# Kernel optimization log

Measured on AMD Instinct MI355X. Metric: run time of the kernel, lower is better.

Reference implementation:

```python
import jax, jax.numpy as jnp
import numpy as np
from jax import lax


def setup_inputs() -> dict:
    key = jax.random.key(0)
    kw, ku, kk, kv = jax.random.split(key, 4)
    B, H, W, C = 8, 16, 16, 256
    # w is a positive per-channel decay (offset keeps exp(sum relu(...)) numerically sane);
    # k, u scaled down like trained RWKV params to avoid exp overflow in the reference.
    w = jax.random.uniform(kw, (C,), dtype=jnp.float32) + 0.3
    u = jax.random.normal(ku, (C,), dtype=jnp.float32) * 0.1
    k = jax.random.normal(kk, (B, H, W, C), dtype=jnp.float32) * 0.1
    v = jax.random.normal(kv, (B, H, W, C), dtype=jnp.float32)
    return {"B": B, "H": H, "W": W, "C": C, "w": w, "u": u, "k": k, "v": v}


def _wkv2d(B, H, W, C, w, u, k, v):
    # kernel covers the whole feature map
    K = 2 * (max(H, W) - 1) + 1
    pad = K // 2
    c = K // 2
    # Manhattan-distance decay weights, (C, K, K), with bonus u at the center.
    coords = jnp.arange(K)
    dist = (jnp.abs(coords[None, :] - c) + jnp.abs(coords[:, None] - c)).astype(w.dtype)
    wmat = -dist[None, :, :] * w[:, None, None]
    wmat = wmat.at[:, c, c].add(u)
    wflat = wmat.reshape(C, K * K).T  # (K*K, C)

    k_chw = jnp.transpose(k, (0, 3, 1, 2))  # (B,C,H,W)
    k_pad = jnp.pad(k_chw, ((0, 0), (0, 0), (pad, pad), (pad, pad)))  # zero pad == F.unfold padding

    idx = jnp.arange(K * K, dtype=jnp.int32)
    dys, dxs = idx // K, idx % K

    # Fused windowed relu-sum: never materialize the (B,C,K^2,HW) unfold tensor.
    def body(acc, xs):
        dy, dx, wc = xs
        win = lax.dynamic_slice(k_pad, (0, 0, dy, dx), (B, C, H, W))
        return acc + jax.nn.relu(win + wc[None, :, None, None]), None

    acc0 = jnp.zeros((B, C, H, W), dtype=k.dtype)
    k_adj, _ = lax.scan(body, acc0, (dys, dxs, wflat))

    v_chw = jnp.transpose(v, (0, 3, 1, 2))
    out = jnp.exp(k_adj) * v_chw  # (B,C,H,W)
    return jnp.transpose(out, (0, 2, 3, 1))  # back to (B,H,W,C)


def reference(B, H, W, C, w, u, k, v):
    return _wkv2d(B, H, W, C, w, u, k, v)
```

## Files before the change

kernel.cpp:

```cpp
#include <hip/hip_runtime.h>
#include <math.h>


constexpr int Bq = 8, Hq = 16, Wq = 16, Cq = 256;
constexpr int HW = Hq * Wq;
constexpr int CG = 16;
constexpr int YT = 2;
constexpr int ROWP = HW + 4;

__global__ __launch_bounds__(256, 4)
void wkv2d_kernel(const float* __restrict__ w,
                  const float* __restrict__ u,
                  const float* __restrict__ k,
                  const float* __restrict__ v,
                  float* __restrict__ out) {
    __shared__ float klds[CG][ROWP];

    const int bid = blockIdx.x;
    const int y0  = (bid & 7) * YT;
    const int c0  = ((bid >> 3) & 15) * CG;
    const int b   = bid >> 7;

    const int tid = threadIdx.x;
    const int cl  = tid & 15;
    const int x   = tid >> 4;

    {
        #pragma unroll
        for (int i = 0; i < 4; ++i) {
            const int f = tid + 256 * i;
            const int p = f >> 2;
            const int q = f & 3;
            const float4 kv = ((const float4*)(k + ((size_t)(b * HW + p)) * Cq + c0))[q];
            klds[4 * q + 0][p] = kv.x;
            klds[4 * q + 1][p] = kv.y;
            klds[4 * q + 2][p] = kv.z;
            klds[4 * q + 3][p] = kv.w;
        }
    }
    __syncthreads();

    const int   c  = c0 + cl;
    const float wc = w[c];
    const float fx = (float)x;
    const float fy0 = (float)y0;

    float wxv[16];
    #pragma unroll
    for (int rx = 0; rx < 16; ++rx)
        wxv[rx] = fabsf((float)rx - fx) * wc;

    float acc0 = 0.f, acc1 = 0.f;
    const float* krow = &klds[cl][0];

    #pragma unroll
    for (int ry = 0; ry < 16; ++ry) {
        const float fy  = (float)ry;
        const float wy0 = fabsf(fy - fy0) * wc;
        const float wy1 = fabsf(fy - fy0 - 1.0f) * wc;

        const float4* rr = (const float4*)(krow + ry * 16);
        #pragma unroll
        for (int j = 0; j < 4; ++j) {
            const float4 r = rr[j];
            const float rv[4] = {r.x, r.y, r.z, r.w};
            #pragma unroll
            for (int t = 0; t < 4; ++t) {
                const float t0 = rv[t] - wxv[4 * j + t];
                acc0 += fmaxf(t0 - wy0, 0.f);
                acc1 += fmaxf(t0 - wy1, 0.f);
            }
        }
    }

    const float uc  = u[c];
    const float ks0 = krow[(y0 + 0) * 16 + x];
    const float ks1 = krow[(y0 + 1) * 16 + x];
    const float a0 = acc0 + fmaxf(ks0 + uc, 0.f) - fmaxf(ks0, 0.f);
    const float a1 = acc1 + fmaxf(ks1 + uc, 0.f) - fmaxf(ks1, 0.f);

    const size_t idx0 = ((size_t)((b * 16 + y0) * 16 + x)) * Cq + c;
    const size_t idx1 = idx0 + (size_t)Wq * Cq;
    out[idx0] = __expf(a0) * v[idx0];
    out[idx1] = __expf(a1) * v[idx1];
}

extern "C" void kernel_launch(void* const* d_in, const int* in_sizes, int n_in,
                              void* d_out, int out_size, void* d_ws, size_t ws_size,
                              hipStream_t stream) {
    const float* w = (const float*)d_in[4];
    const float* u = (const float*)d_in[5];
    const float* k = (const float*)d_in[6];
    const float* v = (const float*)d_in[7];
    float* out = (float*)d_out;

    const int grid = Bq * (Cq / CG) * (Hq / YT);
    wkv2d_kernel<<<grid, 256, 0, stream>>>(w, u, k, v, out);
}
```

Before: 81.62 us.

## Skip zero relu terms by bounding window radius from per-channel k max

Computes the max k per channel in the block and derives the largest Manhattan distance D at which relu(k - d*w) can be positive. When D is small, only a (2D+2)x(2D+1) neighbourhood is summed instead of the whole 16x16 map; otherwise it falls back to the full loop. This cuts ALU work that contributes only zeros, at the cost of an extra reduction, two block barriers and data-dependent, less-unrolled loops.

```diff
diff --git a/kernel.cpp b/kernel.cpp
--- a/kernel.cpp
+++ b/kernel.cpp
@@ -15,6 +15,8 @@
                   const float* __restrict__ v,
                   float* __restrict__ out) {
     __shared__ float klds[CG][ROWP];
+    __shared__ float pmax[CG][17];
+    __shared__ int   sD[CG];
 
     const int bid = blockIdx.x;
     const int y0  = (bid & 7) * YT;
@@ -40,35 +42,88 @@
     }
     __syncthreads();
 
+    {
+        const float4* rr = (const float4*)(&klds[cl][x * 16]);
+        const float4 a = rr[0], bb = rr[1], cc = rr[2], dd = rr[3];
+        float m = fmaxf(fmaxf(fmaxf(a.x, a.y), fmaxf(a.z, a.w)),
+                        fmaxf(fmaxf(bb.x, bb.y), fmaxf(bb.z, bb.w)));
+        m = fmaxf(m, fmaxf(fmaxf(cc.x, cc.y), fmaxf(cc.z, cc.w)));
+        m = fmaxf(m, fmaxf(fmaxf(dd.x, dd.y), fmaxf(dd.z, dd.w)));
+        pmax[cl][x] = m;
+    }
+    __syncthreads();
+
+    if (tid < CG) {
+        float km = pmax[tid][0];
+        #pragma unroll
+        for (int i = 1; i < 16; ++i) km = fmaxf(km, pmax[tid][i]);
+        const float wcc = w[c0 + tid];
+        int D = -1;
+        for (int d = 0; d <= 30; ++d) {
+            if (km > (float)d * wcc - 1e-5f) D = d; else break;
+        }
+        sD[tid] = D;
+    }
+    __syncthreads();
+
+    int Dblk = sD[0];
+    #pragma unroll
+    for (int i = 1; i < 16; ++i) Dblk = max(Dblk, sD[i]);
+
     const int   c  = c0 + cl;
     const float wc = w[c];
     const float fx = (float)x;
     const float fy0 = (float)y0;
 
-    float wxv[16];
-    #pragma unroll
-    for (int rx = 0; rx < 16; ++rx)
-        wxv[rx] = fabsf((float)rx - fx) * wc;
-
     float acc0 = 0.f, acc1 = 0.f;
     const float* krow = &klds[cl][0];
 
-    #pragma unroll
-    for (int ry = 0; ry < 16; ++ry) {
-        const float fy  = (float)ry;
-        const float wy0 = fabsf(fy - fy0) * wc;
-        const float wy1 = fabsf(fy - fy0 - 1.0f) * wc;
+    if (Dblk < 0) {
+    } else if (Dblk <= 5) {
+        const int R = Dblk;
+        const int ry_lo = max(y0 - R, 0);
+        const int ry_hi = min(y0 + 1 + R, 15);
+        for (int ry = ry_lo; ry <= ry_hi; ++ry) {
+            const float fy  = (float)ry;
+            const float wy0 = fabsf(fy - fy0) * wc;
+            const float wy1 = fabsf(fy - fy0 - 1.0f) * wc;
+            const float* kr = krow + ry * 16;
+            for (int i = 0; i <= 2 * R; ++i) {
+                const int rx = x - R + i;
+                const bool ok = ((unsigned)rx < 16u);
+                const int rxc = ok ? rx : 0;
+                const float s  = kr[rxc];
+                const float wx = fabsf((float)rx - fx) * wc;
+                const float t0 = s - wx;
+                const float m0 = fmaxf(t0 - wy0, 0.f);
+                const float m1 = fmaxf(t0 - wy1, 0.f);
+                acc0 += ok ? m0 : 0.f;
+                acc1 += ok ? m1 : 0.f;
+            }
+        }
+    } else {
+        float wxv[16];
+        #pragma unroll
+        for (int rx = 0; rx < 16; ++rx)
+            wxv[rx] = fabsf((float)rx - fx) * wc;
 
-        const float4* rr = (const float4*)(krow + ry * 16);
         #pragma unroll
-        for (int j = 0; j < 4; ++j) {
-            const float4 r = rr[j];
-            const float rv[4] = {r.x, r.y, r.z, r.w};
+        for (int ry = 0; ry < 16; ++ry) {
+            const float fy  = (float)ry;
+            const float wy0 = fabsf(fy - fy0) * wc;
+            const float wy1 = fabsf(fy - fy0 - 1.0f) * wc;
+
+            const float4* rr = (const float4*)(krow + ry * 16);
             #pragma unroll
-            for (int t = 0; t < 4; ++t) {
-                const float t0 = rv[t] - wxv[4 * j + t];
-                acc0 += fmaxf(t0 - wy0, 0.f);
-                acc1 += fmaxf(t0 - wy1, 0.f);
+            for (int j = 0; j < 4; ++j) {
+                const float4 r = rr[j];
+                const float rv[4] = {r.x, r.y, r.z, r.w};
+                #pragma unroll
+                for (int t = 0; t < 4; ++t) {
+                    const float t0 = rv[t] - wxv[4 * j + t];
+                    acc0 += fmaxf(t0 - wy0, 0.f);
+                    acc1 += fmaxf(t0 - wy1, 0.f);
+                }
             }
         }
     }
```

Result: faster. 75.10 us (-8.0%).
